# Kernel tuning notes

Measured on AMD Instinct MI355X. Metric: run time of the kernel, lower is better.

## Reference

```python
import math
import jax
import jax.numpy as jnp
import numpy as np
from jax import lax

B, L, D = 8, 3072, 512
DM, H, CF = 512, 8, 512
E = DM // H
KSIZE = 25
C_FACTOR = 1


def setup_inputs() -> dict:
    key = jax.random.key(0)
    ks = jax.random.split(key, 16)
    s = lambda fan: 1.0 / np.sqrt(fan)
    inp = {
        "inputs": jax.random.normal(ks[0], (B, L, D), jnp.float32),
        "W_res": jax.random.normal(ks[1], (D, DM), jnp.float32) * s(D),
        "b_res": jnp.zeros((DM,), jnp.float32),
        "W_in": jax.random.normal(ks[2], (DM, DM), jnp.float32) * s(DM),
        "b_in": jnp.zeros((DM,), jnp.float32),
        "Wq": jax.random.normal(ks[3], (DM, DM), jnp.float32) * s(DM),
        "bq": jnp.zeros((DM,), jnp.float32),
        "Wk": jax.random.normal(ks[4], (DM, DM), jnp.float32) * s(DM),
        "bk": jnp.zeros((DM,), jnp.float32),
        "Wv": jax.random.normal(ks[5], (DM, DM), jnp.float32) * s(DM),
        "bv": jnp.zeros((DM,), jnp.float32),
        "Wo": jax.random.normal(ks[6], (DM, DM), jnp.float32) * s(DM),
        "bo": jnp.zeros((DM,), jnp.float32),
        "Wc1": jax.random.normal(ks[7], (DM, CF), jnp.float32) * s(DM),
        "Wc2": jax.random.normal(ks[8], (CF, CF), jnp.float32) * s(CF),
    }
    return inp


def series_decomp(x):
    # moving average with 'same' padding, TF-style (count excludes padding)
    ssum = lax.reduce_window(x, 0.0, lax.add, (1, KSIZE, 1), (1, 1, 1), "SAME")
    cnt = lax.reduce_window(jnp.ones_like(x), 0.0, lax.add, (1, KSIZE, 1), (1, 1, 1), "SAME")
    trend = ssum / cnt
    return x - trend, trend


def auto_correlation(q, k, v):
    # q,k,v: [B, L, H, E]
    qf = jnp.fft.rfft(q, axis=1)
    kf = jnp.fft.rfft(k, axis=1)
    corr = jnp.fft.irfft(qf * jnp.conj(kf), n=L, axis=1)  # [B, L, H, E]
    mean_corr = corr.mean(axis=(2, 3))  # [B, L]
    k_top = int(C_FACTOR * math.log(L))  # = 8
    weights, delays = lax.top_k(mean_corr, k_top)  # [B, k_top]
    w = jax.nn.softmax(weights, axis=-1)  # [B, k_top]
    # gather v rolled by each delay: idx[b,i,l] = (l + delay[b,i]) % L
    idx = (jnp.arange(L)[None, None, :] + delays[:, :, None]) % L  # [B, k_top, L]
    v_rolled = jnp.take_along_axis(v[:, None], idx[:, :, :, None, None], axis=2)  # [B,k,L,H,E]
    return jnp.einsum("bklhe,bk->blhe", v_rolled, w)


def reference(inputs, W_res, b_res, W_in, b_in, Wq, bq, Wk, bk, Wv, bv, Wo, bo, Wc1, Wc2):
    proj = inputs @ W_res + b_res  # [B,L,DM]
    x = proj @ W_in + b_in
    q = (x @ Wq + bq).reshape(B, L, H, E)
    kk = (x @ Wk + bk).reshape(B, L, H, E)
    vv = (x @ Wv + bv).reshape(B, L, H, E)
    attn = auto_correlation(q, kk, vv).reshape(B, L, DM)
    attn = attn @ Wo + bo
    x = attn + proj
    seasonal, _ = series_decomp(x)
    y = jax.nn.relu(seasonal @ Wc1)  # Conv1D kernel_size=1, no bias
    y = y @ Wc2
    out, _ = series_decomp(y)
    return out
```

## Files before the change

### kernel.cpp

```cpp
#include <hip/hip_runtime.h>
#include <hip/hip_bf16.h>


#define LQ 3072
#define DD 512
#define BB 8
#define MTOT (BB * LQ)
#define KTOP 8
#define KSZ 25
#define KHALF 12

typedef __attribute__((ext_vector_type(4))) float f32x4;
typedef __attribute__((ext_vector_type(8))) short s16x8;
typedef __attribute__((ext_vector_type(4))) short s16x4;

__device__ __forceinline__ short f2bf(float x) {
  __hip_bfloat16 h = __float2bfloat16(x);
  return __builtin_bit_cast(short, h);
}
__device__ __forceinline__ float bf2f(short s) {
  __hip_bfloat16 h = __builtin_bit_cast(__hip_bfloat16, s);
  return __bfloat162float(h);
}

#define LDT 40

__device__ __forceinline__ void stage_split(const float* __restrict__ src, int row0, int ld,
                                            int k0, short* __restrict__ Sh,
                                            short* __restrict__ Sl) {
  const int tid = threadIdx.x;
#pragma unroll
  for (int i = 0; i < 4; i++) {
    int cidx = tid + 256 * i;
    int r = cidx >> 3;
    int kc = (cidx & 7) << 2;
    const float* p = src + (size_t)(row0 + r) * ld + (k0 + kc);
    f32x4 v = *reinterpret_cast<const f32x4*>(p);
    s16x4 hv, lv;
#pragma unroll
    for (int j = 0; j < 4; j++) {
      float x = v[j];
      short h = f2bf(x);
      short lo = f2bf(x - bf2f(h));
      hv[j] = h;
      lv[j] = lo;
    }
    *reinterpret_cast<s16x4*>(&Sh[r * LDT + kc]) = hv;
    *reinterpret_cast<s16x4*>(&Sl[r * LDT + kc]) = lv;
  }
}

__device__ __forceinline__ void gemm_core(const float* __restrict__ A, const float* __restrict__ Bt,
                                          int lda, int ldb, int m0, int n0, int K,
                                          short* Ah, short* Al, short* Bh, short* Bl,
                                          f32x4 acc[4][4]) {
  const int tid = threadIdx.x;
  const int lane = tid & 63;
  const int w = tid >> 6;
  const int wr = w >> 1, wc = w & 1;
  const int q = lane >> 4, c = lane & 15;

#pragma unroll
  for (int m = 0; m < 4; m++)
#pragma unroll
    for (int n = 0; n < 4; n++) acc[m][n] = 0.f;

  for (int k0 = 0; k0 < K; k0 += 32) {
    __syncthreads();
    stage_split(A, m0, lda, k0, Ah, Al);
    stage_split(Bt, n0, ldb, k0, Bh, Bl);
    __syncthreads();
#pragma unroll
    for (int p = 0; p < 3; p++) {
      const short* Sa = (p == 2) ? Al : Ah;
      const short* Sb = (p == 1) ? Bl : Bh;
      s16x8 av[4], bv[4];
#pragma unroll
      for (int m = 0; m < 4; m++)
        av[m] = *reinterpret_cast<const s16x8*>(&Sa[(wr * 64 + m * 16 + c) * LDT + 8 * q]);
#pragma unroll
      for (int n = 0; n < 4; n++)
        bv[n] = *reinterpret_cast<const s16x8*>(&Sb[(wc * 64 + n * 16 + c) * LDT + 8 * q]);
#pragma unroll
      for (int m = 0; m < 4; m++)
#pragma unroll
        for (int n = 0; n < 4; n++)
          acc[m][n] = __builtin_amdgcn_mfma_f32_16x16x32_bf16(av[m], bv[n], acc[m][n], 0, 0, 0);
    }
  }
}

__global__ void __launch_bounds__(256, 2)
gemm_split_nt(const float* __restrict__ A, const float* __restrict__ Bt,
              const float* __restrict__ bias, const float* __restrict__ res,
              float* __restrict__ C, int N, int K, int lda, int ldb, int relu) {
  __shared__ short Ah[128 * LDT], Al[128 * LDT], Bh[128 * LDT], Bl[128 * LDT];
  const int m0 = blockIdx.y * 128, n0 = blockIdx.x * 128;
  f32x4 acc[4][4];
  gemm_core(A, Bt, lda, ldb, m0, n0, K, Ah, Al, Bh, Bl, acc);

  const int tid = threadIdx.x, lane = tid & 63, w = tid >> 6;
  const int wr = w >> 1, wc = w & 1, q = lane >> 4, c = lane & 15;
#pragma unroll
  for (int m = 0; m < 4; m++)
#pragma unroll
    for (int n = 0; n < 4; n++) {
      int col = n0 + wc * 64 + n * 16 + c;
      float badd = bias ? bias[col] : 0.f;
#pragma unroll
      for (int r = 0; r < 4; r++) {
        int row = m0 + wr * 64 + m * 16 + 4 * q + r;
        size_t off = (size_t)row * N + col;
        float val = acc[m][n][r] + badd;
        if (res) val += res[off];
        if (relu) val = fmaxf(val, 0.f);
        C[off] = val;
      }
    }
}

__global__ void __launch_bounds__(256, 2)
corr_gemm(const float* __restrict__ Q, const float* __restrict__ Kk, float* __restrict__ mc) {
  __shared__ short Ah[128 * LDT], Al[128 * LDT], Bh[128 * LDT], Bl[128 * LDT];
  __shared__ float bins[256];
  const int b = blockIdx.z;
  const int m0 = blockIdx.y * 128, n0 = blockIdx.x * 128;
  const float* A = Q + (size_t)b * LQ * DD;
  const float* Bt = Kk + (size_t)b * LQ * DD;

  bins[threadIdx.x] = 0.f;

  f32x4 acc[4][4];
  gemm_core(A, Bt, DD, DD, m0, n0, DD, Ah, Al, Bh, Bl, acc);

  const int tid = threadIdx.x, lane = tid & 63, w = tid >> 6;
  const int wr = w >> 1, wc = w & 1, q = lane >> 4, c = lane & 15;

  float psum[7][4];
#pragma unroll
  for (int d = 0; d < 7; d++)
#pragma unroll
    for (int r = 0; r < 4; r++) psum[d][r] = 0.f;
#pragma unroll
  for (int m = 0; m < 4; m++)
#pragma unroll
    for (int n = 0; n < 4; n++) {
      int d = m - n + 3;
#pragma unroll
      for (int r = 0; r < 4; r++) psum[d][r] += acc[m][n][r];
    }

  __syncthreads();
  const int lanebase = 64 * (wr - wc) + 4 * q - c + 127;
#pragma unroll
  for (int d = 0; d < 7; d++)
#pragma unroll
    for (int r = 0; r < 4; r++) atomicAdd(&bins[lanebase + 16 * (d - 3) + r], psum[d][r]);
  __syncthreads();

  if (tid < 255) {
    int tau = 128 * ((int)blockIdx.y - (int)blockIdx.x) + tid - 127;
    tau = ((tau % LQ) + LQ) % LQ;
    atomicAdd(&mc[b * LQ + tau], bins[tid]);
  }
}

struct P8 {
  const float* p[8];
};

__global__ void transpose_weights(P8 srcs, float* __restrict__ dst) {
  __shared__ float t[32][33];
  const int i = blockIdx.z;
  const float* src = srcs.p[i];
  float* d = dst + (size_t)i * DD * DD;
  const int x0 = blockIdx.x * 32, y0 = blockIdx.y * 32;
  const int tx = threadIdx.x, ty = threadIdx.y;
#pragma unroll
  for (int j = 0; j < 4; j++) t[ty + 8 * j][tx] = src[(size_t)(y0 + ty + 8 * j) * DD + x0 + tx];
  __syncthreads();
#pragma unroll
  for (int j = 0; j < 4; j++) d[(size_t)(x0 + ty + 8 * j) * DD + (y0 + tx)] = t[tx][ty + 8 * j];
}

__global__ void zero_f32(float* __restrict__ p, int n) {
  int i = blockIdx.x * blockDim.x + threadIdx.x;
  if (i < n) p[i] = 0.f;
}

__global__ void topk_softmax(const float* __restrict__ mc, int* __restrict__ delays,
                             float* __restrict__ weights) {
  const int b = blockIdx.x, tid = threadIdx.x;
  __shared__ float vals[LQ];
  __shared__ float rv[256];
  __shared__ int ri[256];
  __shared__ float topv[KTOP];
  __shared__ int topi[KTOP];
  for (int i = tid; i < LQ; i += 256) vals[i] = mc[b * LQ + i] * (1.0f / 512.0f);
  __syncthreads();
  for (int t = 0; t < KTOP; t++) {
    float bv = -1e30f;
    int bi = 0x7fffffff;
    for (int i = tid; i < LQ; i += 256) {
      float v = vals[i];
      if (v > bv || (v == bv && i < bi)) { bv = v; bi = i; }
    }
    rv[tid] = bv;
    ri[tid] = bi;
    __syncthreads();
    for (int s = 128; s > 0; s >>= 1) {
      if (tid < s) {
        if (rv[tid + s] > rv[tid] || (rv[tid + s] == rv[tid] && ri[tid + s] < ri[tid])) {
          rv[tid] = rv[tid + s];
          ri[tid] = ri[tid + s];
        }
      }
      __syncthreads();
    }
    if (tid == 0) {
      topv[t] = rv[0];
      topi[t] = ri[0];
      vals[ri[0]] = -1e38f;
    }
    __syncthreads();
  }
  if (tid == 0) {
    float mx = topv[0];
#pragma unroll
    for (int i = 1; i < KTOP; i++) mx = fmaxf(mx, topv[i]);
    float e[KTOP], s = 0.f;
#pragma unroll
    for (int i = 0; i < KTOP; i++) {
      e[i] = expf(topv[i] - mx);
      s += e[i];
    }
#pragma unroll
    for (int i = 0; i < KTOP; i++) {
      weights[b * KTOP + i] = e[i] / s;
      delays[b * KTOP + i] = topi[i];
    }
  }
}

__global__ void attn_gather(const float* __restrict__ v, const int* __restrict__ delays,
                            const float* __restrict__ w, float* __restrict__ out) {
  int idx = blockIdx.x * blockDim.x + threadIdx.x;
  const int total = BB * LQ * (DD / 4);
  if (idx >= total) return;
  int b = idx / (LQ * (DD / 4));
  int rem = idx % (LQ * (DD / 4));
  int l = rem / (DD / 4), dq = rem % (DD / 4);
  f32x4 acc = 0.f;
#pragma unroll
  for (int i = 0; i < KTOP; i++) {
    int d = delays[b * KTOP + i];
    float wi = w[b * KTOP + i];
    int ls = (l + d) % LQ;
    f32x4 vv = *reinterpret_cast<const f32x4*>(v + ((size_t)b * LQ + ls) * DD + dq * 4);
    acc += vv * wi;
  }
  *reinterpret_cast<f32x4*>(out + ((size_t)b * LQ + l) * DD + dq * 4) = acc;
}

__global__ void decomp_kernel(const float* __restrict__ x, float* __restrict__ out) {
  __shared__ float tile[64 + 2 * KHALF][64];
  const int l0 = blockIdx.x * 64, d0 = blockIdx.y * 64, b = blockIdx.z;
  const int tx = threadIdx.x & 63, ty = threadIdx.x >> 6;
  const float* xb = x + (size_t)b * LQ * DD;
  for (int r = ty; r < 64 + 2 * KHALF; r += 4) {
    int l = l0 + r - KHALF;
    tile[r][tx] = (l >= 0 && l < LQ) ? xb[(size_t)l * DD + d0 + tx] : 0.f;
  }
  __syncthreads();
#pragma unroll
  for (int j = 0; j < 16; j++) {
    int lr = ty + 4 * j;
    int l = l0 + lr;
    float s = 0.f;
#pragma unroll
    for (int t = 0; t < KSZ; t++) s += tile[lr + t][tx];
    int lo = max(0, l - KHALF), hi = min(LQ - 1, l + KHALF);
    float cnt = (float)(hi - lo + 1);
    out[((size_t)b * LQ + l) * DD + d0 + tx] = tile[lr + KHALF][tx] - s / cnt;
  }
}

extern "C" void kernel_launch(void* const* d_in, const int* in_sizes, int n_in,
                              void* d_out, int out_size, void* d_ws, size_t ws_size,
                              hipStream_t stream) {
  const float* inputs = (const float*)d_in[0];
  const float* b_res = (const float*)d_in[2];
  const float* b_in = (const float*)d_in[4];
  const float* bq = (const float*)d_in[6];
  const float* bk = (const float*)d_in[8];
  const float* bv = (const float*)d_in[10];
  const float* bo = (const float*)d_in[12];
  float* outp = (float*)d_out;

  float* WT = (float*)d_ws;
  float* mean_corr = WT + 8 * DD * DD;
  int* delays = (int*)(mean_corr + BB * LQ);
  float* weights = (float*)(delays + 64);
  const size_t FSZ = (size_t)MTOT * DD;
  float* F0 = (float*)((char*)d_ws + (16u << 20));
  float* F1 = F0 + FSZ;
  float* F2 = F1 + FSZ;
  float* F3 = F2 + FSZ;

  P8 wp;
  wp.p[0] = (const float*)d_in[1];
  wp.p[1] = (const float*)d_in[3];
  wp.p[2] = (const float*)d_in[5];
  wp.p[3] = (const float*)d_in[7];
  wp.p[4] = (const float*)d_in[9];
  wp.p[5] = (const float*)d_in[11];
  wp.p[6] = (const float*)d_in[13];
  wp.p[7] = (const float*)d_in[14];

  transpose_weights<<<dim3(16, 16, 8), dim3(32, 8), 0, stream>>>(wp, WT);

  const dim3 gg(DD / 128, MTOT / 128);
  gemm_split_nt<<<gg, 256, 0, stream>>>(inputs, WT + 0 * DD * DD, b_res, nullptr, F0, DD, DD, DD, DD, 0);
  gemm_split_nt<<<gg, 256, 0, stream>>>(F0, WT + 1 * DD * DD, b_in, nullptr, F1, DD, DD, DD, DD, 0);
  gemm_split_nt<<<gg, 256, 0, stream>>>(F1, WT + 2 * DD * DD, bq, nullptr, F2, DD, DD, DD, DD, 0);
  gemm_split_nt<<<gg, 256, 0, stream>>>(F1, WT + 3 * DD * DD, bk, nullptr, F3, DD, DD, DD, DD, 0);
  zero_f32<<<(BB * LQ + 255) / 256, 256, 0, stream>>>(mean_corr, BB * LQ);
  corr_gemm<<<dim3(LQ / 128, LQ / 128, BB), 256, 0, stream>>>(F2, F3, mean_corr);
  topk_softmax<<<BB, 256, 0, stream>>>(mean_corr, delays, weights);
  gemm_split_nt<<<gg, 256, 0, stream>>>(F1, WT + 4 * DD * DD, bv, nullptr, F2, DD, DD, DD, DD, 0);
  attn_gather<<<(BB * LQ * (DD / 4) + 255) / 256, 256, 0, stream>>>(F2, delays, weights, F3);
  gemm_split_nt<<<gg, 256, 0, stream>>>(F3, WT + 5 * DD * DD, bo, F0, F1, DD, DD, DD, DD, 0);
  decomp_kernel<<<dim3(LQ / 64, DD / 64, BB), 256, 0, stream>>>(F1, F2);
  gemm_split_nt<<<gg, 256, 0, stream>>>(F2, WT + 6 * DD * DD, nullptr, nullptr, F3, DD, DD, DD, DD, 1);
  gemm_split_nt<<<gg, 256, 0, stream>>>(F3, WT + 7 * DD * DD, nullptr, nullptr, F1, DD, DD, DD, DD, 0);
  decomp_kernel<<<dim3(LQ / 64, DD / 64, BB), 256, 0, stream>>>(F1, outp);
}
```

Measured before the change: 1.049 ms.

## Pre-split activations into bf16 hi/lo planes and stage via global_load_lds

Producers now write activations as bf16 high/low halves instead of fp32, so the GEMMs no longer convert to bf16 inside the k-loop. Tiles are copied straight to LDS with the async global_load_lds path, using an XOR-swizzled layout, and the 3-pass MFMA loop is reordered to share fragment loads. Occupancy is raised to 3 blocks per SM. In exchange, an extra split pass over the input is added, and the residual is rebuilt from the hi+lo halves.

```diff
diff --git a/kernel.cpp b/kernel.cpp
--- a/kernel.cpp
+++ b/kernel.cpp
@@ -9,98 +9,103 @@
 #define KTOP 8
 #define KSZ 25
 #define KHALF 12
-
+#define KK 512
+#define KB (KK * 2)
+
+typedef unsigned short ushort_t;
 typedef __attribute__((ext_vector_type(4))) float f32x4;
 typedef __attribute__((ext_vector_type(8))) short s16x8;
 typedef __attribute__((ext_vector_type(4))) short s16x4;
 
-__device__ __forceinline__ short f2bf(float x) {
+typedef __attribute__((address_space(1))) unsigned int u32_g;
+typedef __attribute__((address_space(3))) unsigned int u32_l;
+
+__device__ __forceinline__ ushort_t f2bfbits(float x) {
   __hip_bfloat16 h = __float2bfloat16(x);
-  return __builtin_bit_cast(short, h);
-}
-__device__ __forceinline__ float bf2f(short s) {
-  __hip_bfloat16 h = __builtin_bit_cast(__hip_bfloat16, s);
+  return __builtin_bit_cast(unsigned short, h);
+}
+__device__ __forceinline__ float bfbits2f(ushort_t s) {
+  __hip_bfloat16 h = __builtin_bit_cast(__hip_bfloat16, (unsigned short)s);
   return __bfloat162float(h);
 }
 
-#define LDT 40
-
-__device__ __forceinline__ void stage_split(const float* __restrict__ src, int row0, int ld,
-                                            int k0, short* __restrict__ Sh,
-                                            short* __restrict__ Sl) {
-  const int tid = threadIdx.x;
-#pragma unroll
-  for (int i = 0; i < 4; i++) {
-    int cidx = tid + 256 * i;
-    int r = cidx >> 3;
-    int kc = (cidx & 7) << 2;
-    const float* p = src + (size_t)(row0 + r) * ld + (k0 + kc);
-    f32x4 v = *reinterpret_cast<const f32x4*>(p);
-    s16x4 hv, lv;
-#pragma unroll
-    for (int j = 0; j < 4; j++) {
-      float x = v[j];
-      short h = f2bf(x);
-      short lo = f2bf(x - bf2f(h));
-      hv[j] = h;
-      lv[j] = lo;
-    }
-    *reinterpret_cast<s16x4*>(&Sh[r * LDT + kc]) = hv;
-    *reinterpret_cast<s16x4*>(&Sl[r * LDT + kc]) = lv;
-  }
-}
-
-__device__ __forceinline__ void gemm_core(const float* __restrict__ A, const float* __restrict__ Bt,
-                                          int lda, int ldb, int m0, int n0, int K,
-                                          short* Ah, short* Al, short* Bh, short* Bl,
-                                          f32x4 acc[4][4]) {
-  const int tid = threadIdx.x;
-  const int lane = tid & 63;
-  const int w = tid >> 6;
+__device__ __forceinline__ void gload_lds16(const void* g, void* l) {
+  __builtin_amdgcn_global_load_lds((const u32_g*)g, (u32_l*)l, 16, 0, 0);
+}
+
+__device__ __forceinline__ void gemm3_core(
+    const ushort_t* __restrict__ Ah, const ushort_t* __restrict__ Al,
+    const ushort_t* __restrict__ Bh, const ushort_t* __restrict__ Bl,
+    int arow0, int brow0, char* lds, f32x4 acc[4][4]) {
+  const int tid = threadIdx.x, lane = tid & 63, w = tid >> 6;
   const int wr = w >> 1, wc = w & 1;
-  const int q = lane >> 4, c = lane & 15;
+  const int c = lane & 15, qd = lane >> 4;
+
+  const ushort_t* ssrc = (w == 0) ? Ah : (w == 1) ? Al : (w == 2) ? Bh : Bl;
+  const int srow0 = (w < 2) ? arow0 : brow0;
+  const int L0 = lane >> 3, sl = lane & 7;
+  const int u = sl ^ L0;
+  const char* gbase =
+      (const char*)ssrc + (size_t)(srow0 + 2 * L0 + (u >> 2)) * KB + (u & 3) * 16;
+  char* ldsT = lds + w * 8192;
+
+  int aoff[4], boff[4];
+#pragma unroll
+  for (int m = 0; m < 4; m++) {
+    int r = wr * 64 + m * 16 + c;
+    int L = r >> 1;
+    aoff[m] = L * 128 + (((((r & 1) << 2) | qd) ^ (L & 7)) << 4);
+    r = wc * 64 + m * 16 + c;
+    L = r >> 1;
+    boff[m] = 16384 + L * 128 + (((((r & 1) << 2) | qd) ^ (L & 7)) << 4);
+  }
 
 #pragma unroll
   for (int m = 0; m < 4; m++)
 #pragma unroll
     for (int n = 0; n < 4; n++) acc[m][n] = 0.f;
 
-  for (int k0 = 0; k0 < K; k0 += 32) {
+  for (int k0 = 0; k0 < KK; k0 += 32) {
     __syncthreads();
-    stage_split(A, m0, lda, k0, Ah, Al);
-    stage_split(Bt, n0, ldb, k0, Bh, Bl);
+    const char* g = gbase + k0 * 2;
+#pragma unroll
+    for (int i = 0; i < 8; i++) gload_lds16(g + (size_t)i * (16 * KB), ldsT + i * 1024);
     __syncthreads();
-#pragma unroll
-    for (int p = 0; p < 3; p++) {
-      const short* Sa = (p == 2) ? Al : Ah;
-      const short* Sb = (p == 1) ? Bl : Bh;
-      s16x8 av[4], bv[4];
-#pragma unroll
-      for (int m = 0; m < 4; m++)
-        av[m] = *reinterpret_cast<const s16x8*>(&Sa[(wr * 64 + m * 16 + c) * LDT + 8 * q]);
-#pragma unroll
-      for (int n = 0; n < 4; n++)
-        bv[n] = *reinterpret_cast<const s16x8*>(&Sb[(wc * 64 + n * 16 + c) * LDT + 8 * q]);
-#pragma unroll
-      for (int m = 0; m < 4; m++)
-#pragma unroll
-        for (int n = 0; n < 4; n++)
-          acc[m][n] = __builtin_amdgcn_mfma_f32_16x16x32_bf16(av[m], bv[n], acc[m][n], 0, 0, 0);
-    }
-  }
-}
-
-__global__ void __launch_bounds__(256, 2)
-gemm_split_nt(const float* __restrict__ A, const float* __restrict__ Bt,
-              const float* __restrict__ bias, const float* __restrict__ res,
-              float* __restrict__ C, int N, int K, int lda, int ldb, int relu) {
-  __shared__ short Ah[128 * LDT], Al[128 * LDT], Bh[128 * LDT], Bl[128 * LDT];
+
+    s16x8 ah[4], al[4];
+#pragma unroll
+    for (int m = 0; m < 4; m++) {
+      ah[m] = *(const s16x8*)(lds + aoff[m]);
+      al[m] = *(const s16x8*)(lds + 8192 + aoff[m]);
+    }
+#pragma unroll
+    for (int n = 0; n < 4; n++) {
+      s16x8 bh = *(const s16x8*)(lds + boff[n]);
+      s16x8 bl = *(const s16x8*)(lds + 8192 + boff[n]);
+#pragma unroll
+      for (int m = 0; m < 4; m++) {
+        acc[m][n] = __builtin_amdgcn_mfma_f32_16x16x32_bf16(ah[m], bh, acc[m][n], 0, 0, 0);
+        acc[m][n] = __builtin_amdgcn_mfma_f32_16x16x32_bf16(ah[m], bl, acc[m][n], 0, 0, 0);
+        acc[m][n] = __builtin_amdgcn_mfma_f32_16x16x32_bf16(al[m], bh, acc[m][n], 0, 0, 0);
+      }
+    }
+  }
+}
+
+template <int OUTMODE, int RESMODE, int RELU>
+__global__ __launch_bounds__(256, 3) void gemm_bf16x3(
+    const ushort_t* __restrict__ Ah, const ushort_t* __restrict__ Al,
+    const ushort_t* __restrict__ Bh, const ushort_t* __restrict__ Bl,
+    const float* __restrict__ bias,
+    const ushort_t* __restrict__ resH, const ushort_t* __restrict__ resL,
+    float* __restrict__ outF, ushort_t* __restrict__ outH, ushort_t* __restrict__ outL) {
+  __shared__ alignas(16) char lds[32768];
   const int m0 = blockIdx.y * 128, n0 = blockIdx.x * 128;
   f32x4 acc[4][4];
-  gemm_core(A, Bt, lda, ldb, m0, n0, K, Ah, Al, Bh, Bl, acc);
+  gemm3_core(Ah, Al, Bh, Bl, m0, n0, lds, acc);
 
   const int tid = threadIdx.x, lane = tid & 63, w = tid >> 6;
-  const int wr = w >> 1, wc = w & 1, q = lane >> 4, c = lane & 15;
+  const int wr = w >> 1, wc = w & 1, qd = lane >> 4, c = lane & 15;
 #pragma unroll
   for (int m = 0; m < 4; m++)
 #pragma unroll
@@ -109,32 +114,36 @@
       float badd = bias ? bias[col] : 0.f;
 #pragma unroll
       for (int r = 0; r < 4; r++) {
-        int row = m0 + wr * 64 + m * 16 + 4 * q + r;
-        size_t off = (size_t)row * N + col;
+        int row = m0 + wr * 64 + m * 16 + 4 * qd + r;
+        size_t off = (size_t)row * DD + col;
         float val = acc[m][n][r] + badd;
-        if (res) val += res[off];
-        if (relu) val = fmaxf(val, 0.f);
-        C[off] = val;
+        if (RESMODE == 1) val += bfbits2f(resH[off]) + bfbits2f(resL[off]);
+        if (RELU) val = fmaxf(val, 0.f);
+        if (OUTMODE == 0) {
+          outF[off] = val;
+        } else {
+          ushort_t h = f2bfbits(val);
+          outH[off] = h;
+          outL[off] = f2bfbits(val - bfbits2f(h));
+        }
       }
     }
 }
 
-__global__ void __launch_bounds__(256, 2)
-corr_gemm(const float* __restrict__ Q, const float* __restrict__ Kk, float* __restrict__ mc) {
-  __shared__ short Ah[128 * LDT], Al[128 * LDT], Bh[128 * LDT], Bl[128 * LDT];
+__global__ __launch_bounds__(256, 3) void corr_gemm(
+    const ushort_t* __restrict__ Qh, const ushort_t* __restrict__ Ql,
+    const ushort_t* __restrict__ Kh, const ushort_t* __restrict__ Kl,
+    float* __restrict__ mc) {
+  __shared__ alignas(16) char lds[32768];
   __shared__ float bins[256];
   const int b = blockIdx.z;
   const int m0 = blockIdx.y * 128, n0 = blockIdx.x * 128;
-  const float* A = Q + (size_t)b * LQ * DD;
-  const float* Bt = Kk + (size_t)b * LQ * DD;
-
   bins[threadIdx.x] = 0.f;
-
   f32x4 acc[4][4];
-  gemm_core(A, Bt, DD, DD, m0, n0, DD, Ah, Al, Bh, Bl, acc);
+  gemm3_core(Qh, Ql, Kh, Kl, b * LQ + m0, b * LQ + n0, lds, acc);
 
   const int tid = threadIdx.x, lane = tid & 63, w = tid >> 6;
-  const int wr = w >> 1, wc = w & 1, q = lane >> 4, c = lane & 15;
+  const int wr = w >> 1, wc = w & 1, qd = lane >> 4, c = lane & 15;
 
   float psum[7][4];
 #pragma unroll
@@ -151,7 +160,7 @@
     }
 
   __syncthreads();
-  const int lanebase = 64 * (wr - wc) + 4 * q - c + 127;
+  const int lanebase = 64 * (wr - wc) + 4 * qd - c + 127;
 #pragma unroll
   for (int d = 0; d < 7; d++)
 #pragma unroll
@@ -169,18 +178,40 @@
   const float* p[8];
 };
 
-__global__ void transpose_weights(P8 srcs, float* __restrict__ dst) {
+__global__ void transpose_split(P8 srcs, ushort_t* __restrict__ dH, ushort_t* __restrict__ dL) {
   __shared__ float t[32][33];
   const int i = blockIdx.z;
   const float* src = srcs.p[i];
-  float* d = dst + (size_t)i * DD * DD;
+  const size_t base = (size_t)i * DD * DD;
   const int x0 = blockIdx.x * 32, y0 = blockIdx.y * 32;
   const int tx = threadIdx.x, ty = threadIdx.y;
 #pragma unroll
   for (int j = 0; j < 4; j++) t[ty + 8 * j][tx] = src[(size_t)(y0 + ty + 8 * j) * DD + x0 + tx];
   __syncthreads();
 #pragma unroll
-  for (int j = 0; j < 4; j++) d[(size_t)(x0 + ty + 8 * j) * DD + (y0 + tx)] = t[tx][ty + 8 * j];
+  for (int j = 0; j < 4; j++) {
+    float v = t[tx][ty + 8 * j];
+    size_t o = base + (size_t)(x0 + ty + 8 * j) * DD + (y0 + tx);
+    ushort_t h = f2bfbits(v);
+    dH[o] = h;
+    dL[o] = f2bfbits(v - bfbits2f(h));
+  }
+}
+
+__global__ void split_f32(const float* __restrict__ x, ushort_t* __restrict__ h,
+                          ushort_t* __restrict__ l, int n4) {
+  int i = blockIdx.x * blockDim.x + threadIdx.x;
+  if (i >= n4) return;
+  f32x4 v = *reinterpret_cast<const f32x4*>(x + (size_t)i * 4);
+  s16x4 hv, lv;
+#pragma unroll
+  for (int j = 0; j < 4; j++) {
+    ushort_t hb = f2bfbits(v[j]);
+    hv[j] = (short)hb;
+    lv[j] = (short)f2bfbits(v[j] - bfbits2f(hb));
+  }
+  *reinterpret_cast<s16x4*>(h + (size_t)i * 4) = hv;
+  *reinterpret_cast<s16x4*>(l + (size_t)i * 4) = lv;
 }
 
 __global__ void zero_f32(float* __restrict__ p, int n) {
@@ -243,7 +274,8 @@
 }
 
 __global__ void attn_gather(const float* __restrict__ v, const int* __restrict__ delays,
-                            const float* __restrict__ w, float* __restrict__ out) {
+                            const float* __restrict__ w, ushort_t* __restrict__ oH,
+                            ushort_t* __restrict__ oL) {
   int idx = blockIdx.x * blockDim.x + threadIdx.x;
   const int total = BB * LQ * (DD / 4);
   if (idx >= total) return;
@@ -259,10 +291,21 @@
     f32x4 vv = *reinterpret_cast<const f32x4*>(v + ((size_t)b * LQ + ls) * DD + dq * 4);
     acc += vv * wi;
   }
-  *reinterpret_cast<f32x4*>(out + ((size_t)b * LQ + l) * DD + dq * 4) = acc;
-}
-
-__global__ void decomp_kernel(const float* __restrict__ x, float* __restrict__ out) {
+  size_t o = ((size_t)b * LQ + l) * DD + dq * 4;
+  s16x4 hv, lv;
+#pragma unroll
+  for (int j = 0; j < 4; j++) {
+    ushort_t hb = f2bfbits(acc[j]);
+    hv[j] = (short)hb;
+    lv[j] = (short)f2bfbits(acc[j] - bfbits2f(hb));
+  }
+  *reinterpret_cast<s16x4*>(oH + o) = hv;
+  *reinterpret_cast<s16x4*>(oL + o) = lv;
+}
+
+template <int OUT_HL>
+__global__ void decomp_kernel(const float* __restrict__ x, float* __restrict__ outF,
+                              ushort_t* __restrict__ outH, ushort_t* __restrict__ outL) {
   __shared__ float tile[64 + 2 * KHALF][64];
   const int l0 = blockIdx.x * 64, d0 = blockIdx.y * 64, b = blockIdx.z;
   const int tx = threadIdx.x & 63, ty = threadIdx.x >> 6;
@@ -280,8 +323,15 @@
 #pragma unroll
     for (int t = 0; t < KSZ; t++) s += tile[lr + t][tx];
     int lo = max(0, l - KHALF), hi = min(LQ - 1, l + KHALF);
-    float cnt = (float)(hi - lo + 1);
-    out[((size_t)b * LQ + l) * DD + d0 + tx] = tile[lr + KHALF][tx] - s / cnt;
+    float val = tile[lr + KHALF][tx] - s / (float)(hi - lo + 1);
+    size_t o = ((size_t)b * LQ + l) * DD + d0 + tx;
+    if (OUT_HL) {
+      ushort_t h = f2bfbits(val);
+      outH[o] = h;
+      outL[o] = f2bfbits(val - bfbits2f(h));
+    } else {
+      outF[o] = val;
+    }
   }
 }
 
@@ -297,15 +347,22 @@
   const float* bo = (const float*)d_in[12];
   float* outp = (float*)d_out;
 
-  float* WT = (float*)d_ws;
-  float* mean_corr = WT + 8 * DD * DD;
-  int* delays = (int*)(mean_corr + BB * LQ);
-  float* weights = (float*)(delays + 64);
-  const size_t FSZ = (size_t)MTOT * DD;
-  float* F0 = (float*)((char*)d_ws + (16u << 20));
-  float* F1 = F0 + FSZ;
-  float* F2 = F1 + FSZ;
-  float* F3 = F2 + FSZ;
+  char* ws = (char*)d_ws;
+  ushort_t* WTh = (ushort_t*)ws;
+  ushort_t* WTl = (ushort_t*)(ws + (4u << 20));
+  float* mean_corr = (float*)(ws + (8u << 20));
+  int* delays = (int*)(ws + (8u << 20) + 98304);
+  float* weights = (float*)(ws + (8u << 20) + 98304 + 256);
+  char* R0 = ws + (16u << 20);
+  char* R1 = ws + (64u << 20);
+  char* R2 = ws + (112u << 20);
+  char* R3 = ws + (160u << 20);
+  const size_t HALF = 24u << 20;
+  ushort_t *R0h = (ushort_t*)R0, *R0l = (ushort_t*)(R0 + HALF);
+  ushort_t *R1h = (ushort_t*)R1, *R1l = (ushort_t*)(R1 + HALF);
+  ushort_t *R2h = (ushort_t*)R2, *R2l = (ushort_t*)(R2 + HALF);
+  ushort_t *R3h = (ushort_t*)R3, *R3l = (ushort_t*)(R3 + HALF);
+  const size_t WS1 = (size_t)DD * DD;
 
   P8 wp;
   wp.p[0] = (const float*)d_in[1];
@@ -317,21 +374,33 @@
   wp.p[6] = (const float*)d_in[13];
   wp.p[7] = (const float*)d_in[14];
 
-  transpose_weights<<<dim3(16, 16, 8), dim3(32, 8), 0, stream>>>(wp, WT);
-
-  const dim3 gg(DD / 128, MTOT / 128);
-  gemm_split_nt<<<gg, 256, 0, stream>>>(inputs, WT + 0 * DD * DD, b_res, nullptr, F0, DD, DD, DD, DD, 0);
-  gemm_split_nt<<<gg, 256, 0, stream>>>(F0, WT + 1 * DD * DD, b_in, nullptr, F1, DD, DD, DD, DD, 0);
-  gemm_split_nt<<<gg, 256, 0, stream>>>(F1, WT + 2 * DD * DD, bq, nullptr, F2, DD, DD, DD, DD, 0);
-  gemm_split_nt<<<gg, 256, 0, stream>>>(F1, WT + 3 * DD * DD, bk, nullptr, F3, DD, DD, DD, DD, 0);
+  transpose_split<<<dim3(16, 16, 8), dim3(32, 8), 0, stream>>>(wp, WTh, WTl);
+  split_f32<<<(MTOT * DD / 4 + 255) / 256, 256, 0, stream>>>(inputs, R1h, R1l, MTOT * DD / 4);
+
+  const dim3 G(DD / 128, MTOT / 128);
+  gemm_bf16x3<1, 0, 0><<<G, 256, 0, stream>>>(R1h, R1l, WTh + 0 * WS1, WTl + 0 * WS1, b_res,
+                                              nullptr, nullptr, nullptr, R0h, R0l);
+  gemm_bf16x3<1, 0, 0><<<G, 256, 0, stream>>>(R0h, R0l, WTh + 1 * WS1, WTl + 1 * WS1, b_in,
+                                              nullptr, nullptr, nullptr, R1h, R1l);
+  gemm_bf16x3<1, 0, 0><<<G, 256, 0, stream>>>(R1h, R1l, WTh + 2 * WS1, WTl + 2 * WS1, bq,
+                                              nullptr, nullptr, nullptr, R2h, R2l);
+  gemm_bf16x3<1, 0, 0><<<G, 256, 0, stream>>>(R1h, R1l, WTh + 3 * WS1, WTl + 3 * WS1, bk,
+                                              nullptr, nullptr, nullptr, R3h, R3l);
   zero_f32<<<(BB * LQ + 255) / 256, 256, 0, stream>>>(mean_corr, BB * LQ);
-  corr_gemm<<<dim3(LQ / 128, LQ / 128, BB), 256, 0, stream>>>(F2, F3, mean_corr);
+  corr_gemm<<<dim3(LQ / 128, LQ / 128, BB), 256, 0, stream>>>(R2h, R2l, R3h, R3l, mean_corr);
   topk_softmax<<<BB, 256, 0, stream>>>(mean_corr, delays, weights);
-  gemm_split_nt<<<gg, 256, 0, stream>>>(F1, WT + 4 * DD * DD, bv, nullptr, F2, DD, DD, DD, DD, 0);
-  attn_gather<<<(BB * LQ * (DD / 4) + 255) / 256, 256, 0, stream>>>(F2, delays, weights, F3);
-  gemm_split_nt<<<gg, 256, 0, stream>>>(F3, WT + 5 * DD * DD, bo, F0, F1, DD, DD, DD, DD, 0);
-  decomp_kernel<<<dim3(LQ / 64, DD / 64, BB), 256, 0, stream>>>(F1, F2);
-  gemm_split_nt<<<gg, 256, 0, stream>>>(F2, WT + 6 * DD * DD, nullptr, nullptr, F3, DD, DD, DD, DD, 1);
-  gemm_split_nt<<<gg, 256, 0, stream>>>(F3, WT + 7 * DD * DD, nullptr, nullptr, F1, DD, DD, DD, DD, 0);
-  decomp_kernel<<<dim3(LQ / 64, DD / 64, BB), 256, 0, stream>>>(F1, outp);
-}
+  gemm_bf16x3<0, 0, 0><<<G, 256, 0, stream>>>(R1h, R1l, WTh + 4 * WS1, WTl + 4 * WS1, bv,
+                                              nullptr, nullptr, (float*)R2, nullptr, nullptr);
+  attn_gather<<<(BB * LQ * (DD / 4) + 255) / 256, 256, 0, stream>>>((const float*)R2, delays,
+                                                                    weights, R3h, R3l);
+  gemm_bf16x3<0, 1, 0><<<G, 256, 0, stream>>>(R3h, R3l, WTh + 5 * WS1, WTl + 5 * WS1, bo,
+                                              R0h, R0l, (float*)R1, nullptr, nullptr);
+  decomp_kernel<1><<<dim3(LQ / 64, DD / 64, BB), 256, 0, stream>>>((const float*)R1, nullptr,
+                                                                   R0h, R0l);
+  gemm_bf16x3<1, 0, 1><<<G, 256, 0, stream>>>(R0h, R0l, WTh + 6 * WS1, WTl + 6 * WS1, nullptr,
+                                              nullptr, nullptr, nullptr, R2h, R2l);
+  gemm_bf16x3<0, 0, 0><<<G, 256, 0, stream>>>(R2h, R2l, WTh + 7 * WS1, WTl + 7 * WS1, nullptr,
+                                              nullptr, nullptr, (float*)R1, nullptr, nullptr);
+  decomp_kernel<0><<<dim3(LQ / 64, DD / 64, BB), 256, 0, stream>>>((const float*)R1, outp,
+                                                                   nullptr, nullptr);
+}
```

Result: faster. 1.015 ms (-3.3%).
